# Optimization experiments

Hardware: AMD Instinct MI355X
Metric: run time of the kernel (lower is better)

Reference implementation:

```python
import jax, jax.numpy as jnp
import numpy as np

NUM_HEADS = 16
D_MODEL = 1024
D_K = D_MODEL // NUM_HEADS
B, S = 2, 2048


def setup_inputs() -> dict:
    key = jax.random.key(0)
    ks = jax.random.split(key, 10)
    q = jax.random.normal(ks[0], (B, S, D_MODEL), dtype=jnp.float32)
    k = jax.random.normal(ks[1], (B, S, D_MODEL), dtype=jnp.float32)
    v = jax.random.normal(ks[2], (B, S, D_MODEL), dtype=jnp.float32)
    # causal mask, 1 = keep, 0 = masked (masked_fill(mask==0, -1e9))
    mask = jnp.tril(jnp.ones((S, S), dtype=jnp.int32))[None, None, :, :]
    # Linear weights ~ N(0, 0.02); biases left at torch default-ish small uniform
    std = 0.02
    Wq = jax.random.normal(ks[3], (D_MODEL, D_MODEL), dtype=jnp.float32) * std
    Wk = jax.random.normal(ks[4], (D_MODEL, D_MODEL), dtype=jnp.float32) * std
    Wv = jax.random.normal(ks[5], (D_MODEL, D_MODEL), dtype=jnp.float32) * std
    bound = 1.0 / np.sqrt(D_MODEL)
    bq = jax.random.uniform(ks[6], (D_MODEL,), jnp.float32, -bound, bound)
    bk = jax.random.uniform(ks[7], (D_MODEL,), jnp.float32, -bound, bound)
    bv = jax.random.uniform(ks[8], (D_MODEL,), jnp.float32, -bound, bound)
    return {"q": q, "k": k, "v": v, "mask": mask,
            "Wq": Wq, "bq": bq, "Wk": Wk, "bk": bk, "Wv": Wv, "bv": bv}


def reference(q, k, v, mask, Wq, bq, Wk, bk, Wv, bv):
    # projections (torch Linear: x @ W.T + b), split heads -> [B, H, S, Dk]
    def proj(x, W, b):
        y = x @ W.T + b
        return y.reshape(B, S, NUM_HEADS, D_K).transpose(0, 2, 1, 3)

    qh, kh, vh = proj(q, Wq, bq), proj(k, Wk, bk), proj(v, Wv, bv)
    scores = jnp.einsum('bhqd,bhkd->bhqk', qh, kh) / jnp.sqrt(jnp.float32(D_K))
    scores = jnp.where(mask == 0, jnp.float32(-1e9), scores)
    p = jax.nn.softmax(scores, axis=-1)
    # dropout is identity in eval mode
    x = jnp.einsum('bhqk,bhkd->bhqd', p, vh)  # [B, H, S, Dk]
    return x.transpose(0, 2, 1, 3).reshape(B, S, D_MODEL)
```

## Files before the change

kernel.cpp:

```cpp
#include <hip/hip_runtime.h>

#define B_ 2
#define H_ 16
#define S_ 2048
#define DM 1024
#define DK 64
#define NX (4096 * 1024)
#define NW (1024 * 1024)

typedef unsigned short u16;
typedef __attribute__((ext_vector_type(8))) short bf16x8;
typedef __attribute__((ext_vector_type(8))) unsigned short u16x8;
typedef __attribute__((ext_vector_type(4))) unsigned short u16x4;
typedef __attribute__((ext_vector_type(2))) unsigned int u32x2;
typedef __attribute__((ext_vector_type(4))) float f32x4;

__device__ inline u16 f2bf(float f) {
  union { float f; unsigned int u; } c; c.f = f;
  unsigned int u = c.u;
  u += 0x7fffu + ((u >> 16) & 1u);
  return (u16)(u >> 16);
}

__device__ inline u16x8 cvt8(const float* __restrict__ src) {
  const float4 a = *reinterpret_cast<const float4*>(src);
  const float4 b = *reinterpret_cast<const float4*>(src + 4);
  u16x8 r;
  r[0] = f2bf(a.x); r[1] = f2bf(a.y); r[2] = f2bf(a.z); r[3] = f2bf(a.w);
  r[4] = f2bf(b.x); r[5] = f2bf(b.y); r[6] = f2bf(b.z); r[7] = f2bf(b.w);
  return r;
}

__device__ inline void glds16(const u16* g, u16* l) {
  __builtin_amdgcn_global_load_lds(
      (const __attribute__((address_space(1))) unsigned int*)g,
      (__attribute__((address_space(3))) unsigned int*)l, 16, 0, 0);
}

__device__ inline unsigned cvtpk(float lo, float hi) {
  unsigned r;
  asm("v_cvt_pk_bf16_f32 %0, %1, %2" : "=v"(r) : "v"(lo), "v"(hi));
  return r;
}

__global__ __launch_bounds__(256) void cvt_kernel(
    const float* __restrict__ q, const float* __restrict__ k, const float* __restrict__ v,
    const float* __restrict__ Wq, const float* __restrict__ Wk, const float* __restrict__ Wv,
    u16* __restrict__ Xq, u16* __restrict__ Xk, u16* __restrict__ Xv,
    u16* __restrict__ Wqb, u16* __restrict__ Wkb, u16* __restrict__ Wvb)
{
  const int t = blockIdx.y;
  const float* src = (t == 0) ? q : (t == 1) ? k : (t == 2) ? v
                   : (t == 3) ? Wq : (t == 4) ? Wk : Wv;
  u16* dst = (t == 0) ? Xq : (t == 1) ? Xk : (t == 2) ? Xv
           : (t == 3) ? Wqb : (t == 4) ? Wkb : Wvb;
  const int n = (t < 3) ? NX : NW;
  const int idx = (blockIdx.x * 256 + threadIdx.x) * 8;
  if (idx >= n) return;
  *reinterpret_cast<u16x8*>(&dst[idx]) = cvt8(&src[idx]);
}

__global__ __launch_bounds__(256) void proj_kernel(
    const u16* __restrict__ Xq, const u16* __restrict__ Xk, const u16* __restrict__ Xv,
    const u16* __restrict__ Wqb, const u16* __restrict__ Wkb, const u16* __restrict__ Wvb,
    const float* __restrict__ bq, const float* __restrict__ bk, const float* __restrict__ bv,
    u16* __restrict__ Qh, u16* __restrict__ Kh, u16* __restrict__ Vh)
{
  const int bid = blockIdx.x;
  const int xcd = bid & 7;
  const int tt  = bid >> 3;
  const int z   = tt >> 5;
  const int rr  = tt & 31;
  const int by  = xcd * 4 + (rr >> 3);
  const int bj  = rr & 7;

  const u16* X      = (z == 0) ? Xq : (z == 1) ? Xk : Xv;
  const u16* W      = (z == 0) ? Wqb : (z == 1) ? Wkb : Wvb;
  const float* bias = (z == 0) ? bq : (z == 1) ? bk : bv;
  u16* out          = (z == 0) ? Qh : (z == 1) ? Kh : Vh;
  const float scale = (z == 0) ? 0.18033688f : 1.0f;

  __shared__ __align__(16) u16 Xs[128 * 32];
  __shared__ __align__(16) u16 Ws[128 * 32];

  const int tid = threadIdx.x;
  const int lane = tid & 63;
  const int w = tid >> 6;
  const int wy = w >> 1, wx = w & 1;
  const int m0 = by * 128;
  const int n0 = bj * 128;
  const int ml = lane & 15;
  const int qd = lane >> 4;

  f32x4 acc[4][4] = {};

  for (int kb = 0; kb < DM; kb += 32) {
    __syncthreads();
    #pragma unroll
    for (int p = 0; p < 2; ++p) {
      const int c = p * 4 + w;
      const int row = c * 16 + (lane >> 2);
      const int col = kb + (lane & 3) * 8;
      glds16(&X[(size_t)(m0 + row) * DM + col], &Xs[c * 512]);
      glds16(&W[(size_t)(n0 + row) * DM + col], &Ws[c * 512]);
    }
    __syncthreads();
    bf16x8 a[4], bfr[4];
    #pragma unroll
    for (int i = 0; i < 4; ++i)
      a[i] = *reinterpret_cast<const bf16x8*>(&Xs[(wy * 64 + i * 16 + ml) * 32 + qd * 8]);
    #pragma unroll
    for (int j = 0; j < 4; ++j)
      bfr[j] = *reinterpret_cast<const bf16x8*>(&Ws[(wx * 64 + j * 16 + ml) * 32 + qd * 8]);
    #pragma unroll
    for (int i = 0; i < 4; ++i)
      #pragma unroll
      for (int j = 0; j < 4; ++j)
        acc[i][j] = __builtin_amdgcn_mfma_f32_16x16x32_bf16(a[i], bfr[j], acc[i][j], 0, 0, 0);
  }

  #pragma unroll
  for (int j = 0; j < 4; ++j) {
    const int n = n0 + wx * 64 + j * 16 + ml;
    const float badd = bias[n];
    const int h = n >> 6, d = n & 63;
    #pragma unroll
    for (int i = 0; i < 4; ++i) {
      #pragma unroll
      for (int r = 0; r < 4; ++r) {
        const int m = m0 + wy * 64 + i * 16 + qd * 4 + r;
        const int bi = m >> 11, s = m & 2047;
        out[((bi * H_ + h) * S_ + s) * DK + d] = f2bf((acc[i][j][r] + badd) * scale);
      }
    }
  }
}

__global__ __launch_bounds__(256) void transpose_kernel(
    const u16* __restrict__ Vh, u16* __restrict__ Vt)
{
  __shared__ __align__(16) u16 T[64 * 72];
  const int t = threadIdx.x;
  const int st = blockIdx.x, bh = blockIdx.y;
  {
    const int r = t >> 2, c = (t & 3) * 16;
    const u16* src = &Vh[((size_t)bh * S_ + st * 64 + r) * DK + c];
    *reinterpret_cast<u16x8*>(&T[r * 72 + c])     = *reinterpret_cast<const u16x8*>(src);
    *reinterpret_cast<u16x8*>(&T[r * 72 + c + 8]) = *reinterpret_cast<const u16x8*>(src + 8);
  }
  __syncthreads();
  {
    const int d = t >> 2, s0 = (t & 3) * 16;
    u16x8 a, b;
    #pragma unroll
    for (int i = 0; i < 8; ++i) a[i] = T[(s0 + i) * 72 + d];
    #pragma unroll
    for (int i = 0; i < 8; ++i) b[i] = T[(s0 + 8 + i) * 72 + d];
    u16* dst = &Vt[((size_t)bh * DK + d) * S_ + st * 64 + s0];
    *reinterpret_cast<u16x8*>(dst)     = a;
    *reinterpret_cast<u16x8*>(dst + 8) = b;
  }
}

__global__ __launch_bounds__(256) void attn_kernel(
    const u16* __restrict__ Qh, const u16* __restrict__ Kh,
    const u16* __restrict__ Vt, float* __restrict__ out)
{
  __shared__ __align__(16) u16 Ks[2][64 * 64];
  __shared__ __align__(16) u16 Vs[2][64 * 64];
  __shared__ __align__(16) u16 Ps[4][2][16 * 64];

  const int tid  = threadIdx.x;
  const int lane = tid & 63;
  const int w    = tid >> 6;

  const int fid = blockIdx.x;
  const int bh  = (fid & 7) * 4 + ((fid >> 3) & 3);
  const int qt  = 15 - (fid >> 5);
  const int b   = bh >> 4, h = bh & 15;
  const int ml  = lane & 15, qd = lane >> 4;
  const int m7  = ml & 7;
  const int u0  = qd ^ m7;
  const int qh  = qd >> 1, ql = qd & 1;
  const int R0  = qt * 128;
  const int nt  = 2 * qt + 2;

  bf16x8 qa[2][2];
  #pragma unroll
  for (int g = 0; g < 2; ++g)
    #pragma unroll
    for (int ch = 0; ch < 2; ++ch)
      qa[g][ch] = *reinterpret_cast<const bf16x8*>(
          &Qh[((size_t)bh * S_ + R0 + w * 32 + g * 16 + ml) * DK + ch * 32 + qd * 8]);
  asm volatile("s_waitcnt vmcnt(0)" ::: "memory");

  const u16* kb0 = Kh + (size_t)bh * S_ * DK;
  const u16* vb0 = Vt + (size_t)bh * DK * S_;
  const int r0 = tid >> 3, r1 = r0 + 32;
  const int cs = (tid & 7) ^ (r0 & 7);
  const u16* sK0 = kb0 + r0 * DK + cs * 8;
  const u16* sK1 = kb0 + r1 * DK + cs * 8;
  const u16* sV0 = vb0 + (size_t)r0 * S_ + cs * 8;
  const u16* sV1 = vb0 + (size_t)r1 * S_ + cs * 8;

  f32x4 oacc[2][4] = {};
  float lsum[2] = {0.f, 0.f};

  glds16(sK0, &Ks[0][tid * 8]);
  glds16(sK1, &Ks[0][2048 + tid * 8]);
  glds16(sV0, &Vs[0][tid * 8]);
  glds16(sV1, &Vs[0][2048 + tid * 8]);
  sK0 += 4096; sK1 += 4096; sV0 += 64; sV1 += 64;

  int cur = 0;
  for (int t = 0; t < nt; ++t) {
    if (t + 1 < nt) {
      glds16(sK0, &Ks[cur ^ 1][tid * 8]);
      glds16(sK1, &Ks[cur ^ 1][2048 + tid * 8]);
      glds16(sV0, &Vs[cur ^ 1][tid * 8]);
      glds16(sV1, &Vs[cur ^ 1][2048 + tid * 8]);
      sK0 += 4096; sK1 += 4096; sV0 += 64; sV1 += 64;
      asm volatile("s_waitcnt vmcnt(4)" ::: "memory");
    } else {
      asm volatile("s_waitcnt vmcnt(0)" ::: "memory");
    }
    __builtin_amdgcn_s_barrier();
    asm volatile("" ::: "memory");

    const u16* Kb = Ks[cur];
    const u16* Vb = Vs[cur];

    const int d16_0 = (R0 + w * 32 - t * 64) >> 4;
    const int d16_1 = d16_0 + 1;
    const int jtop  = (d16_1 < 3) ? d16_1 : 3;

    if (jtop >= 0) {
      #pragma unroll
      for (int j = 0; j < 4; ++j) {
        if (j > jtop) break;
        const int rk = (j * 16 + ml) * 64;
        const bf16x8 k0 = *reinterpret_cast<const bf16x8*>(&Kb[rk + u0 * 8]);
        const bf16x8 k1 = *reinterpret_cast<const bf16x8*>(&Kb[rk + (u0 ^ 4) * 8]);
        #pragma unroll
        for (int g = 0; g < 2; ++g) {
          const int d16g = d16_0 + g;
          if (j > d16g) continue;
          f32x4 zz = {};
          zz = __builtin_amdgcn_mfma_f32_16x16x32_bf16(k0, qa[g][0], zz, 0, 0, 0);
          zz = __builtin_amdgcn_mfma_f32_16x16x32_bf16(k1, qa[g][1], zz, 0, 0, 0);
          if (j == d16g) {
            #pragma unroll
            for (int r = 0; r < 4; ++r)
              if (qd * 4 + r > ml) zz[r] = -1e30f;
          }
          const float e0 = __builtin_amdgcn_exp2f(zz[0]);
          const float e1 = __builtin_amdgcn_exp2f(zz[1]);
          const float e2 = __builtin_amdgcn_exp2f(zz[2]);
          const float e3 = __builtin_amdgcn_exp2f(zz[3]);
          lsum[g] += (e0 + e1) + (e2 + e3);
          u32x2 pk;
          pk[0] = cvtpk(e0, e1);
          pk[1] = cvtpk(e2, e3);
          *reinterpret_cast<u32x2*>(
              &Ps[w][g][ml * 64 + (((2 * j + qh) ^ m7) * 8) + ql * 4]) = pk;
        }
      }
      #pragma unroll
      for (int g = 0; g < 2; ++g) {
        const int d16g = d16_0 + g;
        if (d16g == 0 || d16g == 2) {
          const int jz = d16g + 1;
          *reinterpret_cast<u32x2*>(
              &Ps[w][g][ml * 64 + (((2 * jz + qh) ^ m7) * 8) + ql * 4]) = (u32x2){0, 0};
        }
      }
      #pragma unroll
      for (int c = 0; c < 2; ++c) {
        const bool use0 = d16_0 >= 2 * c;
        const bool use1 = d16_1 >= 2 * c;
        if (!(use0 | use1)) continue;
        bf16x8 vb[4];
        #pragma unroll
        for (int dj = 0; dj < 4; ++dj)
          vb[dj] = *reinterpret_cast<const bf16x8*>(
              &Vb[(dj * 16 + ml) * 64 + (u0 ^ (c << 2)) * 8]);
        if (use0) {
          const bf16x8 pa = *reinterpret_cast<const bf16x8*>(
              &Ps[w][0][ml * 64 + (u0 ^ (c << 2)) * 8]);
          #pragma unroll
          for (int dj = 0; dj < 4; ++dj)
            oacc[0][dj] = __builtin_amdgcn_mfma_f32_16x16x32_bf16(pa, vb[dj], oacc[0][dj], 0, 0, 0);
        }
        if (use1) {
          const bf16x8 pa = *reinterpret_cast<const bf16x8*>(
              &Ps[w][1][ml * 64 + (u0 ^ (c << 2)) * 8]);
          #pragma unroll
          for (int dj = 0; dj < 4; ++dj)
            oacc[1][dj] = __builtin_amdgcn_mfma_f32_16x16x32_bf16(pa, vb[dj], oacc[1][dj], 0, 0, 0);
        }
      }
    }

    asm volatile("" ::: "memory");
    __builtin_amdgcn_s_barrier();
    asm volatile("" ::: "memory");
    cur ^= 1;
  }

  #pragma unroll
  for (int g = 0; g < 2; ++g) {
    float lg = lsum[g];
    lg += __shfl_xor(lg, 16, 64);
    lg += __shfl_xor(lg, 32, 64);
    #pragma unroll
    for (int r = 0; r < 4; ++r) {
      const float inv = 1.0f / __shfl(lg, qd * 4 + r, 64);
      const int srow = R0 + w * 32 + g * 16 + qd * 4 + r;
      float* op = &out[(size_t)(b * S_ + srow) * DM + h * DK + ml];
      #pragma unroll
      for (int dj = 0; dj < 4; ++dj)
        op[dj * 16] = oacc[g][dj][r] * inv;
    }
  }
}

extern "C" void kernel_launch(void* const* d_in, const int* in_sizes, int n_in,
                              void* d_out, int out_size, void* d_ws, size_t ws_size,
                              hipStream_t stream) {
  const float* q  = (const float*)d_in[0];
  const float* k  = (const float*)d_in[1];
  const float* v  = (const float*)d_in[2];
  const float* Wq = (const float*)d_in[4];
  const float* bq = (const float*)d_in[5];
  const float* Wk = (const float*)d_in[6];
  const float* bk = (const float*)d_in[7];
  const float* Wv = (const float*)d_in[8];
  const float* bv = (const float*)d_in[9];

  u16* Xq  = (u16*)d_ws;
  u16* Xk  = Xq + NX;
  u16* Xv  = Xk + NX;
  u16* Wqb = Xv + NX;
  u16* Wkb = Wqb + NW;
  u16* Wvb = Wkb + NW;
  u16* Qh  = Wvb + NW;
  u16* Kh  = Qh + NX;
  u16* Vh  = Kh + NX;
  u16* Vt  = Xq;

  cvt_kernel<<<dim3(NX / (256 * 8), 6), 256, 0, stream>>>(
      q, k, v, Wq, Wk, Wv, Xq, Xk, Xv, Wqb, Wkb, Wvb);
  proj_kernel<<<dim3(768), 256, 0, stream>>>(
      Xq, Xk, Xv, Wqb, Wkb, Wvb, bq, bk, bv, Qh, Kh, Vh);
  transpose_kernel<<<dim3(S_ / 64, B_ * H_), 256, 0, stream>>>(Vh, Vt);
  attn_kernel<<<dim3(512), 256, 0, stream>>>(
      Qh, Kh, Vt, (float*)d_out);
}
```

Baseline: 207.2 us.

## Double-buffer LDS tiles in QKV projection GEMM to overlap global loads with MFMA

Turns the projection GEMM's shared-memory X and W tiles into ping-pong buffers. The next k-slice is prefetched with direct global-to-LDS loads while the current slice is consumed, and partial vmcnt waits plus raw s_barrier replace the two __syncthreads per iteration. The aim is to hide global load latency behind the MFMA work. It doubles LDS use and depends on hand-placed waitcnt counts being correct for the glds16 instruction count.

```diff
diff --git a/kernel.cpp b/kernel.cpp
--- a/kernel.cpp
+++ b/kernel.cpp
@@ -80,8 +80,8 @@
   u16* out          = (z == 0) ? Qh : (z == 1) ? Kh : Vh;
   const float scale = (z == 0) ? 0.18033688f : 1.0f;
 
-  __shared__ __align__(16) u16 Xs[128 * 32];
-  __shared__ __align__(16) u16 Ws[128 * 32];
+  __shared__ __align__(16) u16 Xs[2][128 * 32];
+  __shared__ __align__(16) u16 Ws[2][128 * 32];
 
   const int tid = threadIdx.x;
   const int lane = tid & 63;
@@ -92,31 +92,54 @@
   const int ml = lane & 15;
   const int qd = lane >> 4;
 
+  const int srow = (lane >> 2);
+  const int scol = (lane & 3) * 8;
+
   f32x4 acc[4][4] = {};
 
+  #pragma unroll
+  for (int p = 0; p < 2; ++p) {
+    const int c = p * 4 + w;
+    const int row = c * 16 + srow;
+    glds16(&X[(size_t)(m0 + row) * DM + scol], &Xs[0][c * 512]);
+    glds16(&W[(size_t)(n0 + row) * DM + scol], &Ws[0][c * 512]);
+  }
+
+  int cur = 0;
   for (int kb = 0; kb < DM; kb += 32) {
-    __syncthreads();
-    #pragma unroll
-    for (int p = 0; p < 2; ++p) {
-      const int c = p * 4 + w;
-      const int row = c * 16 + (lane >> 2);
-      const int col = kb + (lane & 3) * 8;
-      glds16(&X[(size_t)(m0 + row) * DM + col], &Xs[c * 512]);
-      glds16(&W[(size_t)(n0 + row) * DM + col], &Ws[c * 512]);
-    }
-    __syncthreads();
+    if (kb + 32 < DM) {
+      #pragma unroll
+      for (int p = 0; p < 2; ++p) {
+        const int c = p * 4 + w;
+        const int row = c * 16 + srow;
+        const int col = kb + 32 + scol;
+        glds16(&X[(size_t)(m0 + row) * DM + col], &Xs[cur ^ 1][c * 512]);
+        glds16(&W[(size_t)(n0 + row) * DM + col], &Ws[cur ^ 1][c * 512]);
+      }
+      asm volatile("s_waitcnt vmcnt(4)" ::: "memory");
+    } else {
+      asm volatile("s_waitcnt vmcnt(0)" ::: "memory");
+    }
+    __builtin_amdgcn_s_barrier();
+    asm volatile("" ::: "memory");
+
     bf16x8 a[4], bfr[4];
     #pragma unroll
     for (int i = 0; i < 4; ++i)
-      a[i] = *reinterpret_cast<const bf16x8*>(&Xs[(wy * 64 + i * 16 + ml) * 32 + qd * 8]);
+      a[i] = *reinterpret_cast<const bf16x8*>(&Xs[cur][(wy * 64 + i * 16 + ml) * 32 + qd * 8]);
     #pragma unroll
     for (int j = 0; j < 4; ++j)
-      bfr[j] = *reinterpret_cast<const bf16x8*>(&Ws[(wx * 64 + j * 16 + ml) * 32 + qd * 8]);
+      bfr[j] = *reinterpret_cast<const bf16x8*>(&Ws[cur][(wx * 64 + j * 16 + ml) * 32 + qd * 8]);
     #pragma unroll
     for (int i = 0; i < 4; ++i)
       #pragma unroll
       for (int j = 0; j < 4; ++j)
         acc[i][j] = __builtin_amdgcn_mfma_f32_16x16x32_bf16(a[i], bfr[j], acc[i][j], 0, 0, 0);
+
+    asm volatile("" ::: "memory");
+    __builtin_amdgcn_s_barrier();
+    asm volatile("" ::: "memory");
+    cur ^= 1;
   }
 
   #pragma unroll
```

Result: no change. 210.4 us (+1.5%).

## Fuse fp32-to-bf16 conversion and V transpose into projection GEMM

Applied to the files above, without the earlier changes.

Removes the separate conversion kernel. The projection GEMM now loads fp32 inputs and weights directly, converts them to bf16 in registers with packed cvt, and stores them to LDS, with the next K-slice prefetched into registers. It also drops the standalone V transpose kernel: the V projection epilogue writes its output transposed into Vt with 4-wide packed stores. This saves two launches and the bf16 intermediate traffic through global memory, at the cost of twice the global read bytes per GEMM tile and replacing async global-to-LDS loads with register staging.

```diff
diff --git a/kernel.cpp b/kernel.cpp
--- a/kernel.cpp
+++ b/kernel.cpp
@@ -6,13 +6,13 @@
 #define DM 1024
 #define DK 64
 #define NX (4096 * 1024)
-#define NW (1024 * 1024)
 
 typedef unsigned short u16;
 typedef __attribute__((ext_vector_type(8))) short bf16x8;
 typedef __attribute__((ext_vector_type(8))) unsigned short u16x8;
 typedef __attribute__((ext_vector_type(4))) unsigned short u16x4;
 typedef __attribute__((ext_vector_type(2))) unsigned int u32x2;
+typedef __attribute__((ext_vector_type(4))) unsigned int u32x4;
 typedef __attribute__((ext_vector_type(4))) float f32x4;
 
 __device__ inline u16 f2bf(float f) {
@@ -22,15 +22,6 @@
   return (u16)(u >> 16);
 }
 
-__device__ inline u16x8 cvt8(const float* __restrict__ src) {
-  const float4 a = *reinterpret_cast<const float4*>(src);
-  const float4 b = *reinterpret_cast<const float4*>(src + 4);
-  u16x8 r;
-  r[0] = f2bf(a.x); r[1] = f2bf(a.y); r[2] = f2bf(a.z); r[3] = f2bf(a.w);
-  r[4] = f2bf(b.x); r[5] = f2bf(b.y); r[6] = f2bf(b.z); r[7] = f2bf(b.w);
-  return r;
-}
-
 __device__ inline void glds16(const u16* g, u16* l) {
   __builtin_amdgcn_global_load_lds(
       (const __attribute__((address_space(1))) unsigned int*)g,
@@ -43,28 +34,18 @@
   return r;
 }
 
-__global__ __launch_bounds__(256) void cvt_kernel(
-    const float* __restrict__ q, const float* __restrict__ k, const float* __restrict__ v,
+__device__ inline void pub8(u16* d, float4 a, float4 b) {
+  u32x4 r;
+  r[0] = cvtpk(a.x, a.y); r[1] = cvtpk(a.z, a.w);
+  r[2] = cvtpk(b.x, b.y); r[3] = cvtpk(b.z, b.w);
+  *reinterpret_cast<u32x4*>(d) = r;
+}
+
+__global__ __launch_bounds__(256) void proj_kernel(
+    const float* __restrict__ Xq, const float* __restrict__ Xk, const float* __restrict__ Xv,
     const float* __restrict__ Wq, const float* __restrict__ Wk, const float* __restrict__ Wv,
-    u16* __restrict__ Xq, u16* __restrict__ Xk, u16* __restrict__ Xv,
-    u16* __restrict__ Wqb, u16* __restrict__ Wkb, u16* __restrict__ Wvb)
-{
-  const int t = blockIdx.y;
-  const float* src = (t == 0) ? q : (t == 1) ? k : (t == 2) ? v
-                   : (t == 3) ? Wq : (t == 4) ? Wk : Wv;
-  u16* dst = (t == 0) ? Xq : (t == 1) ? Xk : (t == 2) ? Xv
-           : (t == 3) ? Wqb : (t == 4) ? Wkb : Wvb;
-  const int n = (t < 3) ? NX : NW;
-  const int idx = (blockIdx.x * 256 + threadIdx.x) * 8;
-  if (idx >= n) return;
-  *reinterpret_cast<u16x8*>(&dst[idx]) = cvt8(&src[idx]);
-}
-
-__global__ __launch_bounds__(256) void proj_kernel(
-    const u16* __restrict__ Xq, const u16* __restrict__ Xk, const u16* __restrict__ Xv,
-    const u16* __restrict__ Wqb, const u16* __restrict__ Wkb, const u16* __restrict__ Wvb,
     const float* __restrict__ bq, const float* __restrict__ bk, const float* __restrict__ bv,
-    u16* __restrict__ Qh, u16* __restrict__ Kh, u16* __restrict__ Vh)
+    u16* __restrict__ Qh, u16* __restrict__ Kh, u16* __restrict__ Vt)
 {
   const int bid = blockIdx.x;
   const int xcd = bid & 7;
@@ -74,10 +55,9 @@
   const int by  = xcd * 4 + (rr >> 3);
   const int bj  = rr & 7;
 
-  const u16* X      = (z == 0) ? Xq : (z == 1) ? Xk : Xv;
-  const u16* W      = (z == 0) ? Wqb : (z == 1) ? Wkb : Wvb;
+  const float* X    = (z == 0) ? Xq : (z == 1) ? Xk : Xv;
+  const float* W    = (z == 0) ? Wq : (z == 1) ? Wk : Wv;
   const float* bias = (z == 0) ? bq : (z == 1) ? bk : bv;
-  u16* out          = (z == 0) ? Qh : (z == 1) ? Kh : Vh;
   const float scale = (z == 0) ? 0.18033688f : 1.0f;
 
   __shared__ __align__(16) u16 Xs[128 * 32];
@@ -92,19 +72,40 @@
   const int ml = lane & 15;
   const int qd = lane >> 4;
 
+  const int r4 = lane >> 2;
+  const int c8 = (lane & 3) * 8;
+  const float* Xp0 = X + (size_t)(m0 + w * 16 + r4) * DM + c8;
+  const float* Xp1 = X + (size_t)(m0 + (4 + w) * 16 + r4) * DM + c8;
+  const float* Wp0 = W + (size_t)(n0 + w * 16 + r4) * DM + c8;
+  const float* Wp1 = W + (size_t)(n0 + (4 + w) * 16 + r4) * DM + c8;
+  u16* xd0 = &Xs[w * 512 + r4 * 32 + c8];
+  u16* xd1 = &Xs[(4 + w) * 512 + r4 * 32 + c8];
+  u16* wd0 = &Ws[w * 512 + r4 * 32 + c8];
+  u16* wd1 = &Ws[(4 + w) * 512 + r4 * 32 + c8];
+
   f32x4 acc[4][4] = {};
 
+  float4 xa0 = *(const float4*)(Xp0),     xb0 = *(const float4*)(Xp0 + 4);
+  float4 xa1 = *(const float4*)(Xp1),     xb1 = *(const float4*)(Xp1 + 4);
+  float4 wa0 = *(const float4*)(Wp0),     wb0 = *(const float4*)(Wp0 + 4);
+  float4 wa1 = *(const float4*)(Wp1),     wb1 = *(const float4*)(Wp1 + 4);
+
   for (int kb = 0; kb < DM; kb += 32) {
-    __syncthreads();
-    #pragma unroll
-    for (int p = 0; p < 2; ++p) {
-      const int c = p * 4 + w;
-      const int row = c * 16 + (lane >> 2);
-      const int col = kb + (lane & 3) * 8;
-      glds16(&X[(size_t)(m0 + row) * DM + col], &Xs[c * 512]);
-      glds16(&W[(size_t)(n0 + row) * DM + col], &Ws[c * 512]);
-    }
-    __syncthreads();
+    pub8(xd0, xa0, xb0);
+    pub8(xd1, xa1, xb1);
+    pub8(wd0, wa0, wb0);
+    pub8(wd1, wa1, wb1);
+    if (kb + 32 < DM) {
+      const int kn = kb + 32;
+      xa0 = *(const float4*)(Xp0 + kn); xb0 = *(const float4*)(Xp0 + kn + 4);
+      xa1 = *(const float4*)(Xp1 + kn); xb1 = *(const float4*)(Xp1 + kn + 4);
+      wa0 = *(const float4*)(Wp0 + kn); wb0 = *(const float4*)(Wp0 + kn + 4);
+      wa1 = *(const float4*)(Wp1 + kn); wb1 = *(const float4*)(Wp1 + kn + 4);
+    }
+    asm volatile("s_waitcnt lgkmcnt(0)" ::: "memory");
+    __builtin_amdgcn_s_barrier();
+    asm volatile("" ::: "memory");
+
     bf16x8 a[4], bfr[4];
     #pragma unroll
     for (int i = 0; i < 4; ++i)
@@ -117,48 +118,45 @@
       #pragma unroll
       for (int j = 0; j < 4; ++j)
         acc[i][j] = __builtin_amdgcn_mfma_f32_16x16x32_bf16(a[i], bfr[j], acc[i][j], 0, 0, 0);
+
+    asm volatile("" ::: "memory");
+    __builtin_amdgcn_s_barrier();
+    asm volatile("" ::: "memory");
   }
 
-  #pragma unroll
-  for (int j = 0; j < 4; ++j) {
-    const int n = n0 + wx * 64 + j * 16 + ml;
-    const float badd = bias[n];
-    const int h = n >> 6, d = n & 63;
-    #pragma unroll
-    for (int i = 0; i < 4; ++i) {
-      #pragma unroll
-      for (int r = 0; r < 4; ++r) {
-        const int m = m0 + wy * 64 + i * 16 + qd * 4 + r;
-        const int bi = m >> 11, s = m & 2047;
-        out[((bi * H_ + h) * S_ + s) * DK + d] = f2bf((acc[i][j][r] + badd) * scale);
-      }
-    }
-  }
-}
-
-__global__ __launch_bounds__(256) void transpose_kernel(
-    const u16* __restrict__ Vh, u16* __restrict__ Vt)
-{
-  __shared__ __align__(16) u16 T[64 * 72];
-  const int t = threadIdx.x;
-  const int st = blockIdx.x, bh = blockIdx.y;
-  {
-    const int r = t >> 2, c = (t & 3) * 16;
-    const u16* src = &Vh[((size_t)bh * S_ + st * 64 + r) * DK + c];
-    *reinterpret_cast<u16x8*>(&T[r * 72 + c])     = *reinterpret_cast<const u16x8*>(src);
-    *reinterpret_cast<u16x8*>(&T[r * 72 + c + 8]) = *reinterpret_cast<const u16x8*>(src + 8);
-  }
-  __syncthreads();
-  {
-    const int d = t >> 2, s0 = (t & 3) * 16;
-    u16x8 a, b;
-    #pragma unroll
-    for (int i = 0; i < 8; ++i) a[i] = T[(s0 + i) * 72 + d];
-    #pragma unroll
-    for (int i = 0; i < 8; ++i) b[i] = T[(s0 + 8 + i) * 72 + d];
-    u16* dst = &Vt[((size_t)bh * DK + d) * S_ + st * 64 + s0];
-    *reinterpret_cast<u16x8*>(dst)     = a;
-    *reinterpret_cast<u16x8*>(dst + 8) = b;
+  if (z == 2) {
+    #pragma unroll
+    for (int j = 0; j < 4; ++j) {
+      const int n = n0 + wx * 64 + j * 16 + ml;
+      const float badd = bias[n];
+      const int h = n >> 6, d = n & 63;
+      #pragma unroll
+      for (int i = 0; i < 4; ++i) {
+        const int mb = m0 + wy * 64 + i * 16 + qd * 4;
+        const int bi = mb >> 11, s0 = mb & 2047;
+        u16x4 pk4;
+        #pragma unroll
+        for (int r = 0; r < 4; ++r) pk4[r] = f2bf(acc[i][j][r] + badd);
+        *reinterpret_cast<u16x4*>(&Vt[((size_t)(bi * H_ + h) * DK + d) * S_ + s0]) = pk4;
+      }
+    }
+  } else {
+    u16* out = (z == 0) ? Qh : Kh;
+    #pragma unroll
+    for (int j = 0; j < 4; ++j) {
+      const int n = n0 + wx * 64 + j * 16 + ml;
+      const float badd = bias[n];
+      const int h = n >> 6, d = n & 63;
+      #pragma unroll
+      for (int i = 0; i < 4; ++i) {
+        #pragma unroll
+        for (int r = 0; r < 4; ++r) {
+          const int m = m0 + wy * 64 + i * 16 + qd * 4 + r;
+          const int bi = m >> 11, s = m & 2047;
+          out[((bi * H_ + h) * S_ + s) * DK + d] = f2bf((acc[i][j][r] + badd) * scale);
+        }
+      }
+    }
   }
 }
 
@@ -337,22 +335,12 @@
   const float* Wv = (const float*)d_in[8];
   const float* bv = (const float*)d_in[9];
 
-  u16* Xq  = (u16*)d_ws;
-  u16* Xk  = Xq + NX;
-  u16* Xv  = Xk + NX;
-  u16* Wqb = Xv + NX;
-  u16* Wkb = Wqb + NW;
-  u16* Wvb = Wkb + NW;
-  u16* Qh  = Wvb + NW;
-  u16* Kh  = Qh + NX;
-  u16* Vh  = Kh + NX;
-  u16* Vt  = Xq;
-
-  cvt_kernel<<<dim3(NX / (256 * 8), 6), 256, 0, stream>>>(
-      q, k, v, Wq, Wk, Wv, Xq, Xk, Xv, Wqb, Wkb, Wvb);
+  u16* Qh = (u16*)d_ws;
+  u16* Kh = Qh + NX;
+  u16* Vt = Kh + NX;
+
   proj_kernel<<<dim3(768), 256, 0, stream>>>(
-      Xq, Xk, Xv, Wqb, Wkb, Wvb, bq, bk, bv, Qh, Kh, Vh);
-  transpose_kernel<<<dim3(S_ / 64, B_ * H_), 256, 0, stream>>>(Vh, Vt);
+      q, k, v, Wq, Wk, Wv, bq, bk, bv, Qh, Kh, Vt);
   attn_kernel<<<dim3(512), 256, 0, stream>>>(
       Qh, Kh, Vt, (float*)d_out);
 }
```

After: 216.2 us. 4.3% more time.
